# Kernel tuning notes

Measured on AMD Instinct MI355X. Metric: run time of the kernel, lower is better.

The kernel has to match this reference:

```python
import jax, jax.numpy as jnp
import numpy as np

DIM = 1024
NUM_EXPERTS = 8
TOP_K = 2
B, S = 2, 2048
HID = 4 * DIM


def setup_inputs() -> dict:
    key = jax.random.key(0)
    ks = jax.random.split(key, 7)
    scale = 0.02
    x = jax.random.normal(ks[0], (B, S, DIM), dtype=jnp.float32)
    gate_w = jax.random.normal(ks[1], (DIM, NUM_EXPERTS), dtype=jnp.float32) * scale
    gate_b = jnp.zeros((NUM_EXPERTS,), dtype=jnp.float32)
    w1 = jax.random.normal(ks[2], (NUM_EXPERTS, DIM, HID), dtype=jnp.float32) * scale
    b1 = jnp.zeros((NUM_EXPERTS, HID), dtype=jnp.float32)
    w2 = jax.random.normal(ks[3], (NUM_EXPERTS, HID, DIM), dtype=jnp.float32) * scale
    b2 = jnp.zeros((NUM_EXPERTS, DIM), dtype=jnp.float32)
    return {"x": x, "gate_w": gate_w, "gate_b": gate_b,
            "w1": w1, "b1": b1, "w2": w2, "b2": b2}


def reference(x, gate_w, gate_b, w1, b1, w2, b2):
    # Gate: [B,S,E]
    gates = jnp.einsum('bsd,de->bse', x, gate_w) + gate_b
    top_w, top_idx = jax.lax.top_k(gates, TOP_K)          # [B,S,K]
    probs = jax.nn.softmax(top_w, axis=-1)                # softmax over selected logits
    # Dense all-expert FFN (matches original: every expert runs on every token)
    h = jnp.einsum('bsd,edh->bseh', x, w1) + b1           # [B,S,E,4D]
    h = jax.nn.gelu(h, approximate=False)                 # exact GELU (torch default)
    y = jnp.einsum('bseh,ehd->bsed', h, w2) + b2          # [B,S,E,D]
    # Select top-k experts per token and combine
    sel = jnp.take_along_axis(y, top_idx[..., None], axis=2)   # [B,S,K,D]
    return jnp.sum(sel * probs[..., None], axis=2)        # [B,S,D]
```

## Files before the change

kernel.cpp:

```cpp
#include <hip/hip_runtime.h>
#include <hip/hip_bf16.h>

#define T_TOKENS 4096
#define DIM      1024
#define HID      4096
#define NE       8
#define CAP      4096
#define SPLITS   4
#define KSP      (HID / SPLITS)

typedef __attribute__((ext_vector_type(8))) short  bf16x8;
typedef __attribute__((ext_vector_type(4))) float  f32x4;
typedef __attribute__((ext_vector_type(4))) ushort u16x4;

__device__ static inline ushort f2bf(float f) {
    __hip_bfloat16 h = __float2bfloat16(f);
    return *(ushort*)&h;
}

__device__ static inline void gll16(const void* g, void* l) {
    __builtin_amdgcn_global_load_lds(
        (const __attribute__((address_space(1))) void*)g,
        (__attribute__((address_space(3))) void*)l,
        16, 0, 0);
}

#define MFMA16(a, b, c) __builtin_amdgcn_mfma_f32_16x16x32_bf16((a), (b), (c), 0, 0, 0)

__global__ __launch_bounds__(64) void gate_kernel(
    const float* __restrict__ x, const float* __restrict__ gw,
    const float* __restrict__ gb, __hip_bfloat16* __restrict__ xb,
    int* __restrict__ counts, int* __restrict__ tlist, float* __restrict__ plist)
{
    const int tok = blockIdx.x;
    const int l   = threadIdx.x;
    const float* xr = x + (size_t)tok * DIM;

    float part[NE];
#pragma unroll
    for (int e = 0; e < NE; e++) part[e] = 0.f;

#pragma unroll
    for (int i = 0; i < DIM / 64; i++) {
        int d = i * 64 + l;
        float xv = xr[d];
        xb[(size_t)tok * DIM + d] = __float2bfloat16(xv);
        const float4* g4 = (const float4*)(gw + (size_t)d * NE);
        float4 a = g4[0], b = g4[1];
        part[0] += xv * a.x; part[1] += xv * a.y;
        part[2] += xv * a.z; part[3] += xv * a.w;
        part[4] += xv * b.x; part[5] += xv * b.y;
        part[6] += xv * b.z; part[7] += xv * b.w;
    }
#pragma unroll
    for (int off = 32; off > 0; off >>= 1) {
#pragma unroll
        for (int e = 0; e < NE; e++) part[e] += __shfl_xor(part[e], off, 64);
    }
    if (l == 0) {
        float lg[NE];
#pragma unroll
        for (int e = 0; e < NE; e++) lg[e] = part[e] + gb[e];
        int i0 = 0;
#pragma unroll
        for (int e = 1; e < NE; e++) if (lg[e] > lg[i0]) i0 = e;
        int i1 = (i0 == 0) ? 1 : 0;
#pragma unroll
        for (int e = 0; e < NE; e++) if (e != i0 && lg[e] > lg[i1]) i1 = e;
        float t  = expf(lg[i1] - lg[i0]);
        float p0 = 1.f / (1.f + t);
        float p1 = t / (1.f + t);
        int pos0 = atomicAdd(&counts[i0], 1);
        tlist[i0 * CAP + pos0] = tok;              plist[i0 * CAP + pos0] = p0;
        int pos1 = atomicAdd(&counts[i1], 1);
        tlist[i1 * CAP + pos1] = tok | (1 << 15);  plist[i1 * CAP + pos1] = p1;
    }
}

__global__ void finalize_kernel(const int* __restrict__ counts, int* __restrict__ base,
                                int* __restrict__ task1, int* __restrict__ task2,
                                int* __restrict__ ntasks)
{
    __shared__ int stc[NE], so1[NE], so2[NE];
    if (threadIdx.x == 0) {
        int acc = 0, o1 = 0, o2 = 0;
        for (int e = 0; e < NE; e++) {
            base[e] = acc; acc += counts[e];
            int tc = (counts[e] + 255) >> 8;
            stc[e] = tc; so1[e] = o1; so2[e] = o2;
            o1 += tc * 16; o2 += tc * 16;
        }
        base[NE] = acc;
        ntasks[0] = o1; ntasks[1] = o2;
    }
    __syncthreads();
    for (int e = 0; e < NE; e++) {
        int tc = stc[e];
        for (int i = threadIdx.x; i < tc * 16; i += 64) {
            int rb = i >> 4, cb = i & 15;
            task1[so1[e] + i] = (e << 16) | (rb << 8) | cb;
        }
        for (int i = threadIdx.x; i < tc * 16; i += 64) {
            int rb = i >> 4, c = i & 15;
            task2[so2[e] + i] = (e << 16) | (rb << 8) | c;
        }
    }
}

__global__ __launch_bounds__(256) void transpose_cvt64(
    const float* __restrict__ in, __hip_bfloat16* __restrict__ outp, int K, int N)
{
    __shared__ ushort tile[64][68];
    const int e  = blockIdx.z;
    const float* src = in + (size_t)e * K * N;
    ushort* dst = (ushort*)outp + (size_t)e * K * N;
    const int k0 = blockIdx.y * 64, n0 = blockIdx.x * 64;
    const int tid = threadIdx.x;

    const int rn4 = (tid & 15) * 4;
    const int rk  = tid >> 4;
#pragma unroll
    for (int p = 0; p < 4; p++) {
        int k = rk + p * 16;
        float4 v = *(const float4*)&src[(size_t)(k0 + k) * N + n0 + rn4];
        tile[k][rn4 + 0] = f2bf(v.x);
        tile[k][rn4 + 1] = f2bf(v.y);
        tile[k][rn4 + 2] = f2bf(v.z);
        tile[k][rn4 + 3] = f2bf(v.w);
    }
    __syncthreads();
    const int wk4 = (tid & 15) * 4;
    const int wn  = tid >> 4;
#pragma unroll
    for (int p = 0; p < 4; p++) {
        int n = wn + p * 16;
        u16x4 u;
        u[0] = tile[wk4 + 0][n];
        u[1] = tile[wk4 + 1][n];
        u[2] = tile[wk4 + 2][n];
        u[3] = tile[wk4 + 3][n];
        *(u16x4*)&dst[(size_t)(n0 + n) * K + k0 + wk4] = u;
    }
}


#define AOFFc(d,s) (((d)*2+(s))*8192)
#define BOFFc(d,s) (32768 + ((d)*2+(s))*8192)

#define MFMA_CL(nj0, nj1)                                                    \
    _Pragma("unroll")                                                        \
    for (int mi = 0; mi < 8; mi++) {                                         \
        acc[mi][nj0] = MFMA16(af[mi], bf##nj0, acc[mi][nj0]);                \
        acc[mi][nj1] = MFMA16(af[mi], bf##nj1, acc[mi][nj1]);                \
    }

#define GEMM_CORE(NT, srcA0, srcA1, srcB0, srcB1)                            \
    f32x4 acc[8][4];                                                         \
    _Pragma("unroll")                                                        \
    for (int i = 0; i < 8; i++)                                              \
        _Pragma("unroll")                                                    \
        for (int j = 0; j < 4; j++) acc[i][j] = (f32x4){0.f,0.f,0.f,0.f};    \
    const int a0 = (wr * 128 + lm) * 32 + rch;                               \
    const int b0 = (wc * 64 + lm) * 32 + rch;                                \
    gll16(srcA0,      &lds[AOFFc(0,0) + w*512]);                             \
    gll16(srcA1,      &lds[AOFFc(0,0) + 4096 + w*512]);                      \
    gll16(srcB0,      &lds[BOFFc(0,0) + w*512]);                             \
    gll16(srcB1,      &lds[BOFFc(0,0) + 4096 + w*512]);                      \
    gll16(srcA0 + 32, &lds[AOFFc(0,1) + w*512]);                             \
    gll16(srcA1 + 32, &lds[AOFFc(0,1) + 4096 + w*512]);                      \
    gll16(srcB0 + 32, &lds[BOFFc(0,1) + w*512]);                             \
    gll16(srcB1 + 32, &lds[BOFFc(0,1) + 4096 + w*512]);                      \
    asm volatile("s_waitcnt vmcnt(4)" ::: "memory");                         \
    gll16(srcA0 + 64, &lds[AOFFc(1,0) + w*512]);                             \
    gll16(srcA1 + 64, &lds[AOFFc(1,0) + 4096 + w*512]);                      \
    gll16(srcB0 + 64, &lds[BOFFc(1,0) + w*512]);                             \
    gll16(srcB1 + 64, &lds[BOFFc(1,0) + 4096 + w*512]);                      \
    gll16(srcA0 + 96, &lds[AOFFc(1,1) + w*512]);                             \
    gll16(srcA1 + 96, &lds[AOFFc(1,1) + 4096 + w*512]);                      \
    asm volatile("s_waitcnt vmcnt(6)" ::: "memory");                         \
    __builtin_amdgcn_s_barrier();                                            \
    _Pragma("unroll 1")                                                      \
    for (int t = 0; t < NT; t++) {                                           \
        const int d   = t & 1;                                               \
        const int aof  = d * 16384,        bof  = 32768 + d * 16384;         \
        const int bofN = 32768 + (d^1) * 16384;                              \
        bf16x8 af[8]; bf16x8 bf0, bf1, bf2, bf3;                             \
        _Pragma("unroll")                                                    \
        for (int mi = 0; mi < 8; mi++)                                       \
            af[mi] = *(const bf16x8*)&lds[aof + a0 + mi*512];                \
        bf0 = *(const bf16x8*)&lds[bof + b0];                                \
        bf1 = *(const bf16x8*)&lds[bof + b0 + 512];                          \
        if (t + 1 < NT) {                                                    \
            size_t ko = (size_t)(t+1)*64 + 32;                               \
            gll16(srcB0 + ko, &lds[bofN + 8192 + w*512]);                    \
            gll16(srcB1 + ko, &lds[bofN + 8192 + 4096 + w*512]);             \
        }                                                                    \
        __builtin_amdgcn_s_barrier();                                        \
        __builtin_amdgcn_s_setprio(1);                                       \
        MFMA_CL(0, 1)                                                        \
        __builtin_amdgcn_s_setprio(0);                                       \
        __builtin_amdgcn_s_barrier();                                        \
        bf2 = *(const bf16x8*)&lds[bof + b0 + 1024];                         \
        bf3 = *(const bf16x8*)&lds[bof + b0 + 1536];                         \
        if (t + 2 < NT) {                                                    \
            size_t ko = (size_t)(t+2)*64;                                    \
            gll16(srcA0 + ko, &lds[aof + w*512]);                            \
            gll16(srcA1 + ko, &lds[aof + 4096 + w*512]);                     \
        }                                                                    \
        __builtin_amdgcn_s_barrier();                                        \
        __builtin_amdgcn_s_setprio(1);                                       \
        MFMA_CL(2, 3)                                                        \
        __builtin_amdgcn_s_setprio(0);                                       \
        __builtin_amdgcn_s_barrier();                                        \
        _Pragma("unroll")                                                    \
        for (int mi = 0; mi < 8; mi++)                                       \
            af[mi] = *(const bf16x8*)&lds[aof + 8192 + a0 + mi*512];         \
        bf0 = *(const bf16x8*)&lds[bof + 8192 + b0];                         \
        bf1 = *(const bf16x8*)&lds[bof + 8192 + b0 + 512];                   \
        if (t + 2 < NT) {                                                    \
            size_t ko = (size_t)(t+2)*64;                                    \
            gll16(srcB0 + ko, &lds[bof + w*512]);                            \
            gll16(srcB1 + ko, &lds[bof + 4096 + w*512]);                     \
        }                                                                    \
        __builtin_amdgcn_s_barrier();                                        \
        __builtin_amdgcn_s_setprio(1);                                       \
        MFMA_CL(0, 1)                                                        \
        __builtin_amdgcn_s_setprio(0);                                       \
        __builtin_amdgcn_s_barrier();                                        \
        bf2 = *(const bf16x8*)&lds[bof + 8192 + b0 + 1024];                  \
        bf3 = *(const bf16x8*)&lds[bof + 8192 + b0 + 1536];                  \
        if (t + 2 < NT) {                                                    \
            size_t ko = (size_t)(t+2)*64 + 32;                               \
            gll16(srcA0 + ko, &lds[aof + 8192 + w*512]);                     \
            gll16(srcA1 + ko, &lds[aof + 8192 + 4096 + w*512]);              \
        }                                                                    \
        __builtin_amdgcn_s_barrier();                                        \
        __builtin_amdgcn_s_setprio(1);                                       \
        MFMA_CL(2, 3)                                                        \
        __builtin_amdgcn_s_setprio(0);                                       \
        if (t < NT - 2) { asm volatile("s_waitcnt vmcnt(6)" ::: "memory"); } \
        else            { asm volatile("s_waitcnt vmcnt(0)" ::: "memory"); } \
        __builtin_amdgcn_s_barrier();                                        \
    }

#define CORE_IDX                                                             \
    const int tid = threadIdx.x;                                             \
    const int l = tid & 63, w = tid >> 6;                                    \
    const int wr = w >> 2, wc = w & 3;                                       \
    const int lm = l & 15, kg = l >> 4;                                      \
    const int rch = (kg ^ ((lm >> 1) & 3)) * 8;                              \
    const int srow = tid >> 2;                                               \
    const int sch  = tid & 3;                                                \
    const int sc0  = (sch ^ ((srow >> 1) & 3)) * 8;

__global__ __launch_bounds__(512, 1) void ffn1_kernel(
    const __hip_bfloat16* __restrict__ xb, const __hip_bfloat16* __restrict__ w1t,
    const float* __restrict__ b1, const int* __restrict__ counts,
    const int* __restrict__ base, const int* __restrict__ tlist,
    const int* __restrict__ task1, const int* __restrict__ ntasks,
    int* __restrict__ ticket, __hip_bfloat16* __restrict__ H)
{
    __shared__ __align__(16) ushort lds[65536];
    __shared__ int s_task;
    CORE_IDX
    const int nt1 = ntasks[0];

    for (;;) {
        __syncthreads();
        if (tid == 0) s_task = atomicAdd(ticket, 1);
        __syncthreads();
        const int task = s_task;
        if (task >= nt1) break;
        const int v  = task1[task];
        const int e  = v >> 16, rb = (v >> 8) & 255, cb = v & 255;
        const int ne = counts[e];
        const int hb = base[e];

        const int rA0g = rb * 256 + srow;
        const int rA1g = rA0g + 128;
        const int tok0 = tlist[e * CAP + (rA0g < ne ? rA0g : ne - 1)] & 0xFFF;
        const int tok1 = tlist[e * CAP + (rA1g < ne ? rA1g : ne - 1)] & 0xFFF;
        const ushort* srcA0 = (const ushort*)xb + (size_t)tok0 * DIM + sc0;
        const ushort* srcA1 = (const ushort*)xb + (size_t)tok1 * DIM + sc0;
        const ushort* srcB0 = (const ushort*)w1t + ((size_t)e * HID + cb * 256 + srow) * DIM + sc0;
        const ushort* srcB1 = srcB0 + (size_t)128 * DIM;

        GEMM_CORE(16, srcA0, srcA1, srcB0, srcB1)

#pragma unroll
        for (int nj = 0; nj < 4; nj++) {
            int col = wc * 64 + nj * 16 + lm;
            float bias = b1[e * HID + cb * 256 + col];
#pragma unroll
            for (int mi = 0; mi < 8; mi++) {
#pragma unroll
                for (int jj = 0; jj < 4; jj++) {
                    int row = wr * 128 + mi * 16 + kg * 4 + jj;
                    float vv = acc[mi][nj][jj] + bias;
                    vv = 0.5f * vv * (1.0f + erff(vv * 0.70710678118654752f));
                    lds[row * 256 + (col ^ ((row & 12) << 2))] = f2bf(vv);
                }
            }
        }
        __syncthreads();
#pragma unroll
        for (int pch = 0; pch < 16; pch++) {
            int c   = pch * 512 + tid;
            int row = c >> 5, seg = c & 31;
            int r   = rb * 256 + row;
            if (r < ne) {
                int pseg = seg ^ ((row & 12) >> 1);
                bf16x8 vv8 = *(const bf16x8*)&lds[row * 256 + pseg * 8];
                *(bf16x8*)((ushort*)H + (size_t)(hb + r) * HID + cb * 256 + seg * 8) = vv8;
            }
        }
    }
}

__global__ __launch_bounds__(512, 1) void ffn2_kernel(
    const __hip_bfloat16* __restrict__ H, const __hip_bfloat16* __restrict__ w2t,
    const float* __restrict__ b2, const int* __restrict__ counts,
    const int* __restrict__ base, const int* __restrict__ tlist,
    const float* __restrict__ plist, const int* __restrict__ task2,
    const int* __restrict__ ntasks, int* __restrict__ ticket,
    __hip_bfloat16* __restrict__ Y)
{
    __shared__ __align__(16) ushort lds[65536];
    __shared__ int s_task;
    CORE_IDX
    const int nt2 = ntasks[1];

    for (;;) {
        __syncthreads();
        if (tid == 0) s_task = atomicAdd(ticket, 1);
        __syncthreads();
        const int task = s_task;
        if (task >= nt2) break;
        const int v  = task2[task];
        const int e  = v >> 16, rb = (v >> 8) & 255;
        const int c  = v & 255;
        const int cb = c >> 2, sp = c & 3;
        const int ne = counts[e];
        const int hb = base[e];

        const int rA0g = rb * 256 + srow;
        const int rA1g = rA0g + 128;
        const int hr0  = hb + (rA0g < ne ? rA0g : ne - 1);
        const int hr1  = hb + (rA1g < ne ? rA1g : ne - 1);
        const size_t ko0 = (size_t)sp * KSP;
        const ushort* srcA0 = (const ushort*)H + (size_t)hr0 * HID + ko0 + sc0;
        const ushort* srcA1 = (const ushort*)H + (size_t)hr1 * HID + ko0 + sc0;
        const ushort* srcB0 = (const ushort*)w2t + ((size_t)e * DIM + cb * 256 + srow) * HID + ko0 + sc0;
        const ushort* srcB1 = srcB0 + (size_t)128 * HID;

        GEMM_CORE(16, srcA0, srcA1, srcB0, srcB1)

#pragma unroll
        for (int nj = 0; nj < 4; nj++) {
            int col = wc * 64 + nj * 16 + lm;
            float bias = (sp == 0) ? b2[e * DIM + cb * 256 + col] : 0.f;
#pragma unroll
            for (int mi = 0; mi < 8; mi++) {
#pragma unroll
                for (int jj = 0; jj < 4; jj++) {
                    int row = wr * 128 + mi * 16 + kg * 4 + jj;
                    int r   = rb * 256 + row;
                    float p = plist[e * CAP + (r < ne ? r : ne - 1)];
                    float vv = (acc[mi][nj][jj] + bias) * p;
                    lds[row * 256 + (col ^ ((row & 12) << 2))] = f2bf(vv);
                }
            }
        }
        __syncthreads();
#pragma unroll
        for (int pch = 0; pch < 16; pch++) {
            int cch = pch * 512 + tid;
            int row = cch >> 5, seg = cch & 31;
            int r   = rb * 256 + row;
            if (r < ne) {
                int tv  = tlist[e * CAP + r];
                int tok = tv & 0xFFF, kk = tv >> 15;
                int pseg = seg ^ ((row & 12) >> 1);
                bf16x8 vv8 = *(const bf16x8*)&lds[row * 256 + pseg * 8];
                *(bf16x8*)((ushort*)Y + ((size_t)(kk * 4 + sp) * T_TOKENS + tok) * DIM
                           + cb * 256 + seg * 8) = vv8;
            }
        }
    }
}

__global__ __launch_bounds__(256) void reduce_kernel(
    const __hip_bfloat16* __restrict__ Y, float* __restrict__ out)
{
    const size_t i = ((size_t)blockIdx.x * 256 + threadIdx.x) * 8;
    float s[8];
#pragma unroll
    for (int j = 0; j < 8; j++) s[j] = 0.f;
#pragma unroll
    for (int sl = 0; sl < 8; sl++) {
        bf16x8 v = *(const bf16x8*)((const ushort*)Y + (size_t)sl * T_TOKENS * DIM + i);
#pragma unroll
        for (int j = 0; j < 8; j++) {
            union { unsigned int ui; float f; } cv;
            cv.ui = ((unsigned int)(ushort)v[j]) << 16;
            s[j] += cv.f;
        }
    }
#pragma unroll
    for (int j = 0; j < 8; j++) out[i + j] = s[j];
}

extern "C" void kernel_launch(void* const* d_in, const int* in_sizes, int n_in,
                              void* d_out, int out_size, void* d_ws, size_t ws_size,
                              hipStream_t stream)
{
    const float* x  = (const float*)d_in[0];
    const float* gw = (const float*)d_in[1];
    const float* gb = (const float*)d_in[2];
    const float* w1 = (const float*)d_in[3];
    const float* b1 = (const float*)d_in[4];
    const float* w2 = (const float*)d_in[5];
    const float* b2 = (const float*)d_in[6];
    float* out = (float*)d_out;

    char* ws = (char*)d_ws;
    __hip_bfloat16* w1t = (__hip_bfloat16*)(ws);
    __hip_bfloat16* w2t = (__hip_bfloat16*)(ws + 67108864);
    __hip_bfloat16* Hb  = (__hip_bfloat16*)(ws + 134217728);
    __hip_bfloat16* xb  = (__hip_bfloat16*)(ws + 201326592);
    int*   tlist  = (int*)  (ws + 209715200);
    float* plist  = (float*)(ws + 209846272);
    int*   counts = (int*)  (ws + 209977344);
    int*   basep  = (int*)  (ws + 209977408);
    int*   ntasks = (int*)  (ws + 209977472);
    int*   tickets= (int*)  (ws + 209977536);
    int*   task1  = (int*)  (ws + 209977600);
    int*   task2  = (int*)  (ws + 209985792);
    __hip_bfloat16* Y = (__hip_bfloat16*)(ws);

    hipMemsetAsync(counts, 0, 256, stream);

    gate_kernel<<<T_TOKENS, 64, 0, stream>>>(x, gw, gb, xb, counts, tlist, plist);
    finalize_kernel<<<1, 64, 0, stream>>>(counts, basep, task1, task2, ntasks);

    transpose_cvt64<<<dim3(HID / 64, DIM / 64, NE), 256, 0, stream>>>(w1, w1t, DIM, HID);
    transpose_cvt64<<<dim3(DIM / 64, HID / 64, NE), 256, 0, stream>>>(w2, w2t, HID, DIM);

    ffn1_kernel<<<256, 512, 0, stream>>>(
        xb, w1t, b1, counts, basep, tlist, task1, ntasks, &tickets[0], Hb);
    ffn2_kernel<<<256, 512, 0, stream>>>(
        Hb, w2t, b2, counts, basep, tlist, plist, task2, ntasks, &tickets[1], Y);
    reduce_kernel<<<(T_TOKENS * DIM / 8) / 256, 256, 0, stream>>>(Y, out);
}
```

Measured before the change: 462.2 us.

## Pin workgroups to experts with per-expert tickets and column-major task order

Replaces the global task list and single ticket counter with a fixed mapping: each workgroup serves expert blockIdx&7 and draws tasks from a per-expert atomic ticket. Tasks are ordered with the row-block index fastest, so consecutive tasks reuse the same weight column tile across token row blocks, aiming at better L2/MALL reuse of weights. This also drops the task-table construction in finalize. The risk is load imbalance: each expert gets a fixed 32 workgroups regardless of its token count, and workgroups assigned to empty experts exit immediately.

```diff
diff --git a/kernel.cpp b/kernel.cpp
--- a/kernel.cpp
+++ b/kernel.cpp
@@ -77,33 +77,12 @@
     }
 }
 
-__global__ void finalize_kernel(const int* __restrict__ counts, int* __restrict__ base,
-                                int* __restrict__ task1, int* __restrict__ task2,
-                                int* __restrict__ ntasks)
-{
-    __shared__ int stc[NE], so1[NE], so2[NE];
+__global__ void finalize_kernel(const int* __restrict__ counts, int* __restrict__ base)
+{
     if (threadIdx.x == 0) {
-        int acc = 0, o1 = 0, o2 = 0;
-        for (int e = 0; e < NE; e++) {
-            base[e] = acc; acc += counts[e];
-            int tc = (counts[e] + 255) >> 8;
-            stc[e] = tc; so1[e] = o1; so2[e] = o2;
-            o1 += tc * 16; o2 += tc * 16;
-        }
+        int acc = 0;
+        for (int e = 0; e < NE; e++) { base[e] = acc; acc += counts[e]; }
         base[NE] = acc;
-        ntasks[0] = o1; ntasks[1] = o2;
-    }
-    __syncthreads();
-    for (int e = 0; e < NE; e++) {
-        int tc = stc[e];
-        for (int i = threadIdx.x; i < tc * 16; i += 64) {
-            int rb = i >> 4, cb = i & 15;
-            task1[so1[e] + i] = (e << 16) | (rb << 8) | cb;
-        }
-        for (int i = threadIdx.x; i < tc * 16; i += 64) {
-            int rb = i >> 4, c = i & 15;
-            task2[so2[e] + i] = (e << 16) | (rb << 8) | c;
-        }
     }
 }
 
@@ -257,24 +236,25 @@
     const __hip_bfloat16* __restrict__ xb, const __hip_bfloat16* __restrict__ w1t,
     const float* __restrict__ b1, const int* __restrict__ counts,
     const int* __restrict__ base, const int* __restrict__ tlist,
-    const int* __restrict__ task1, const int* __restrict__ ntasks,
-    int* __restrict__ ticket, __hip_bfloat16* __restrict__ H)
+    int* __restrict__ tickets, __hip_bfloat16* __restrict__ H)
 {
     __shared__ __align__(16) ushort lds[65536];
     __shared__ int s_task;
     CORE_IDX
-    const int nt1 = ntasks[0];
+    const int e  = blockIdx.x & 7;
+    const int ne = counts[e];
+    const int tc = (ne + 255) >> 8;
+    const int ntask = tc * 16;
+    const int hb = base[e];
+    if (tc == 0) return;
 
     for (;;) {
         __syncthreads();
-        if (tid == 0) s_task = atomicAdd(ticket, 1);
-        __syncthreads();
-        const int task = s_task;
-        if (task >= nt1) break;
-        const int v  = task1[task];
-        const int e  = v >> 16, rb = (v >> 8) & 255, cb = v & 255;
-        const int ne = counts[e];
-        const int hb = base[e];
+        if (tid == 0) s_task = atomicAdd(&tickets[e], 1);
+        __syncthreads();
+        const int i = s_task;
+        if (i >= ntask) break;
+        const int cb = i / tc, rb = i - cb * tc;
 
         const int rA0g = rb * 256 + srow;
         const int rA1g = rA0g + 128;
@@ -321,27 +301,27 @@
     const __hip_bfloat16* __restrict__ H, const __hip_bfloat16* __restrict__ w2t,
     const float* __restrict__ b2, const int* __restrict__ counts,
     const int* __restrict__ base, const int* __restrict__ tlist,
-    const float* __restrict__ plist, const int* __restrict__ task2,
-    const int* __restrict__ ntasks, int* __restrict__ ticket,
+    const float* __restrict__ plist, int* __restrict__ tickets,
     __hip_bfloat16* __restrict__ Y)
 {
     __shared__ __align__(16) ushort lds[65536];
     __shared__ int s_task;
     CORE_IDX
-    const int nt2 = ntasks[1];
+    const int e  = blockIdx.x & 7;
+    const int ne = counts[e];
+    const int tc = (ne + 255) >> 8;
+    const int ntask = tc * 16;
+    const int hb = base[e];
+    if (tc == 0) return;
 
     for (;;) {
         __syncthreads();
-        if (tid == 0) s_task = atomicAdd(ticket, 1);
-        __syncthreads();
-        const int task = s_task;
-        if (task >= nt2) break;
-        const int v  = task2[task];
-        const int e  = v >> 16, rb = (v >> 8) & 255;
-        const int c  = v & 255;
+        if (tid == 0) s_task = atomicAdd(&tickets[NE + e], 1);
+        __syncthreads();
+        const int i = s_task;
+        if (i >= ntask) break;
+        const int c  = i / tc, rb = i - c * tc;
         const int cb = c >> 2, sp = c & 3;
-        const int ne = counts[e];
-        const int hb = base[e];
 
         const int rA0g = rb * 256 + srow;
         const int rA1g = rA0g + 128;
@@ -432,23 +412,20 @@
     float* plist  = (float*)(ws + 209846272);
     int*   counts = (int*)  (ws + 209977344);
     int*   basep  = (int*)  (ws + 209977408);
-    int*   ntasks = (int*)  (ws + 209977472);
-    int*   tickets= (int*)  (ws + 209977536);
-    int*   task1  = (int*)  (ws + 209977600);
-    int*   task2  = (int*)  (ws + 209985792);
+    int*   tickets= (int*)  (ws + 209977472);
     __hip_bfloat16* Y = (__hip_bfloat16*)(ws);
 
-    hipMemsetAsync(counts, 0, 256, stream);
+    hipMemsetAsync(counts, 0, 192, stream);
 
     gate_kernel<<<T_TOKENS, 64, 0, stream>>>(x, gw, gb, xb, counts, tlist, plist);
-    finalize_kernel<<<1, 64, 0, stream>>>(counts, basep, task1, task2, ntasks);
+    finalize_kernel<<<1, 64, 0, stream>>>(counts, basep);
 
     transpose_cvt64<<<dim3(HID / 64, DIM / 64, NE), 256, 0, stream>>>(w1, w1t, DIM, HID);
     transpose_cvt64<<<dim3(DIM / 64, HID / 64, NE), 256, 0, stream>>>(w2, w2t, HID, DIM);
 
     ffn1_kernel<<<256, 512, 0, stream>>>(
-        xb, w1t, b1, counts, basep, tlist, task1, ntasks, &tickets[0], Hb);
+        xb, w1t, b1, counts, basep, tlist, tickets, Hb);
     ffn2_kernel<<<256, 512, 0, stream>>>(
-        Hb, w2t, b2, counts, basep, tlist, plist, task2, ntasks, &tickets[1], Y);
+        Hb, w2t, b2, counts, basep, tlist, plist, tickets, Y);
     reduce_kernel<<<(T_TOKENS * DIM / 8) / 256, 256, 0, stream>>>(Y, out);
 }
```

Measured after the change: 467.2 us. About the same (+1.1%).
